# Kernel tuning notes

Hardware: AMD Instinct MI355X
Metric: run time of the kernel (lower is better)

The kernel has to match this reference:

```python
import jax, jax.numpy as jnp
import numpy as np

EPS = 1e-08

def setup_inputs() -> dict:
    key = jax.random.key(0)
    k1, k2, k3 = jax.random.split(key, 3)
    B, T, V = 16384, 512, 2
    outputs = jax.random.uniform(k1, (B, T, V), dtype=jnp.float32)
    targets = jax.random.uniform(k2, (B, T, V), dtype=jnp.float32)
    weights = jax.random.uniform(k3, (B, T), dtype=jnp.float32)
    return {"outputs": outputs, "targets": targets, "weights": weights}

def reference(outputs, targets, weights):
    # Faithful vectorization of the double python loop in CensoredLoss_Sub
    # (reduction='mean'). Original accumulates a length-D vector:
    #   loss += (t0 * log(1 - o) + t1 * log(o)) * w  over all (i, t)
    # then returns -loss / (B*T).
    B, T, V = targets.shape
    out = outputs.reshape(B, T, -1)                 # (B, T, D)
    loss1 = targets[:, :, 0:1] * jnp.log((1.0 - out) + EPS)
    loss2 = targets[:, :, 1:2] * jnp.log(out + EPS)
    total = (loss1 + loss2) * weights[:, :, None]   # (B, T, D)
    loss = jnp.sum(total, axis=(0, 1))              # (D,)
    return -loss / (B * T)
```

## Files before the change

kernel.cpp:

```cpp
#include <hip/hip_runtime.h>

#define EPS 1e-8f
#define NBLOCKS 2048
#define NTHREADS 256

__global__ __launch_bounds__(NTHREADS) void cl_partial(
    const float4* __restrict__ o4p,
    const float4* __restrict__ t4p,
    const float2* __restrict__ w2p,
    float* __restrict__ ws,
    int M)
{
    int tid = blockIdx.x * blockDim.x + threadIdx.x;
    int stride = gridDim.x * blockDim.x;

    float s0 = 0.0f, s1 = 0.0f;

    for (int j = tid; j < M; j += stride) {
        float4 o4 = o4p[j];
        float4 t4 = t4p[j];
        float2 w2 = w2p[j];

        float lA0m = __logf((1.0f - o4.x) + EPS);
        float lA0  = __logf(o4.x + EPS);
        float lA1m = __logf((1.0f - o4.y) + EPS);
        float lA1  = __logf(o4.y + EPS);
        s0 += (t4.x * lA0m + t4.y * lA0) * w2.x;
        s1 += (t4.x * lA1m + t4.y * lA1) * w2.x;

        float lB0m = __logf((1.0f - o4.z) + EPS);
        float lB0  = __logf(o4.z + EPS);
        float lB1m = __logf((1.0f - o4.w) + EPS);
        float lB1  = __logf(o4.w + EPS);
        s0 += (t4.z * lB0m + t4.w * lB0) * w2.y;
        s1 += (t4.z * lB1m + t4.w * lB1) * w2.y;
    }

    #pragma unroll
    for (int off = 32; off > 0; off >>= 1) {
        s0 += __shfl_down(s0, off, 64);
        s1 += __shfl_down(s1, off, 64);
    }

    __shared__ float sm[ (NTHREADS/64) * 2 ];
    int wave = threadIdx.x >> 6;
    int lane = threadIdx.x & 63;
    if (lane == 0) { sm[wave * 2 + 0] = s0; sm[wave * 2 + 1] = s1; }
    __syncthreads();

    if (threadIdx.x == 0) {
        float b0 = 0.0f, b1 = 0.0f;
        #pragma unroll
        for (int wv = 0; wv < NTHREADS / 64; ++wv) {
            b0 += sm[wv * 2 + 0];
            b1 += sm[wv * 2 + 1];
        }
        ws[blockIdx.x * 2 + 0] = b0;
        ws[blockIdx.x * 2 + 1] = b1;
    }
}

__global__ __launch_bounds__(NTHREADS) void cl_final(
    const float* __restrict__ ws,
    float* __restrict__ out,
    int nblocks,
    float invN)
{
    double s0 = 0.0, s1 = 0.0;
    for (int j = threadIdx.x; j < nblocks; j += NTHREADS) {
        s0 += (double)ws[j * 2 + 0];
        s1 += (double)ws[j * 2 + 1];
    }

    #pragma unroll
    for (int off = 32; off > 0; off >>= 1) {
        s0 += __shfl_down(s0, off, 64);
        s1 += __shfl_down(s1, off, 64);
    }

    __shared__ double sm[ (NTHREADS/64) * 2 ];
    int wave = threadIdx.x >> 6;
    int lane = threadIdx.x & 63;
    if (lane == 0) { sm[wave * 2 + 0] = s0; sm[wave * 2 + 1] = s1; }
    __syncthreads();

    if (threadIdx.x == 0) {
        double b0 = 0.0, b1 = 0.0;
        #pragma unroll
        for (int wv = 0; wv < NTHREADS / 64; ++wv) {
            b0 += sm[wv * 2 + 0];
            b1 += sm[wv * 2 + 1];
        }
        out[0] = (float)(-b0 * (double)invN);
        out[1] = (float)(-b1 * (double)invN);
    }
}

extern "C" void kernel_launch(void* const* d_in, const int* in_sizes, int n_in,
                              void* d_out, int out_size, void* d_ws, size_t ws_size,
                              hipStream_t stream) {
    const float* outputs = (const float*)d_in[0];
    const float* targets = (const float*)d_in[1];
    const float* weights = (const float*)d_in[2];

    int N = in_sizes[2];
    int M = N / 2;

    float* ws = (float*)d_ws;
    float* out = (float*)d_out;

    int nblocks = (M + NTHREADS - 1) / NTHREADS;
    if (nblocks > NBLOCKS) nblocks = NBLOCKS;

    cl_partial<<<nblocks, NTHREADS, 0, stream>>>(
        (const float4*)outputs, (const float4*)targets, (const float2*)weights,
        ws, M);

    cl_final<<<1, NTHREADS, 0, stream>>>(ws, out, nblocks, 1.0f / (float)N);
}
```

Measured before the change: 34.84 us.

## Use larger grid with two-item-per-thread fast path and upfront loads

Raises the grid cap so that each thread handles exactly two float4 groups. When the problem size matches, all six loads are issued up front behind a scheduling barrier, and the compute follows. Adds an occupancy hint and vectorized float2 reads in the final reduction. This is meant to increase memory-level parallelism and remove grid-stride loop overhead. The cost is more partial sums for the single-block final kernel to reduce.

```diff
diff --git a/kernel.cpp b/kernel.cpp
--- a/kernel.cpp
+++ b/kernel.cpp
@@ -1,39 +1,51 @@
 #include <hip/hip_runtime.h>
 
 #define EPS 1e-8f
-#define NBLOCKS 2048
+#define NBLOCKS 8192
 #define NTHREADS 256
 
-__global__ __launch_bounds__(NTHREADS) void cl_partial(
+__device__ __forceinline__ void accum_group(float4 o4, float4 t4, float2 w2,
+                                            float& s0, float& s1) {
+    float lA0m = __logf((1.0f - o4.x) + EPS);
+    float lA0  = __logf(o4.x + EPS);
+    float lA1m = __logf((1.0f - o4.y) + EPS);
+    float lA1  = __logf(o4.y + EPS);
+    s0 += (t4.x * lA0m + t4.y * lA0) * w2.x;
+    s1 += (t4.x * lA1m + t4.y * lA1) * w2.x;
+    float lB0m = __logf((1.0f - o4.z) + EPS);
+    float lB0  = __logf(o4.z + EPS);
+    float lB1m = __logf((1.0f - o4.w) + EPS);
+    float lB1  = __logf(o4.w + EPS);
+    s0 += (t4.z * lB0m + t4.w * lB0) * w2.y;
+    s1 += (t4.z * lB1m + t4.w * lB1) * w2.y;
+}
+
+__global__ __launch_bounds__(NTHREADS, 8) void cl_partial(
     const float4* __restrict__ o4p,
     const float4* __restrict__ t4p,
     const float2* __restrict__ w2p,
     float* __restrict__ ws,
     int M)
 {
-    int tid = blockIdx.x * blockDim.x + threadIdx.x;
-    int stride = gridDim.x * blockDim.x;
+    int tid = blockIdx.x * NTHREADS + threadIdx.x;
+    int stride = gridDim.x * NTHREADS;
 
     float s0 = 0.0f, s1 = 0.0f;
 
-    for (int j = tid; j < M; j += stride) {
-        float4 o4 = o4p[j];
-        float4 t4 = t4p[j];
-        float2 w2 = w2p[j];
-
-        float lA0m = __logf((1.0f - o4.x) + EPS);
-        float lA0  = __logf(o4.x + EPS);
-        float lA1m = __logf((1.0f - o4.y) + EPS);
-        float lA1  = __logf(o4.y + EPS);
-        s0 += (t4.x * lA0m + t4.y * lA0) * w2.x;
-        s1 += (t4.x * lA1m + t4.y * lA1) * w2.x;
-
-        float lB0m = __logf((1.0f - o4.z) + EPS);
-        float lB0  = __logf(o4.z + EPS);
-        float lB1m = __logf((1.0f - o4.w) + EPS);
-        float lB1  = __logf(o4.w + EPS);
-        s0 += (t4.z * lB0m + t4.w * lB0) * w2.y;
-        s1 += (t4.z * lB1m + t4.w * lB1) * w2.y;
+    if (M == 2 * stride) {
+        float4 oa = o4p[tid];
+        float4 ob = o4p[tid + stride];
+        float4 ta = t4p[tid];
+        float4 tb = t4p[tid + stride];
+        float2 wa = w2p[tid];
+        float2 wb = w2p[tid + stride];
+        __builtin_amdgcn_sched_barrier(0);
+        accum_group(oa, ta, wa, s0, s1);
+        accum_group(ob, tb, wb, s0, s1);
+    } else {
+        for (int j = tid; j < M; j += stride) {
+            accum_group(o4p[j], t4p[j], w2p[j], s0, s1);
+        }
     }
 
     #pragma unroll
@@ -42,7 +54,7 @@
         s1 += __shfl_down(s1, off, 64);
     }
 
-    __shared__ float sm[ (NTHREADS/64) * 2 ];
+    __shared__ float sm[(NTHREADS / 64) * 2];
     int wave = threadIdx.x >> 6;
     int lane = threadIdx.x & 63;
     if (lane == 0) { sm[wave * 2 + 0] = s0; sm[wave * 2 + 1] = s1; }
@@ -61,15 +73,16 @@
 }
 
 __global__ __launch_bounds__(NTHREADS) void cl_final(
-    const float* __restrict__ ws,
+    const float2* __restrict__ ws,
     float* __restrict__ out,
     int nblocks,
     float invN)
 {
     double s0 = 0.0, s1 = 0.0;
     for (int j = threadIdx.x; j < nblocks; j += NTHREADS) {
-        s0 += (double)ws[j * 2 + 0];
-        s1 += (double)ws[j * 2 + 1];
+        float2 p = ws[j];
+        s0 += (double)p.x;
+        s1 += (double)p.y;
     }
 
     #pragma unroll
@@ -78,7 +91,7 @@
         s1 += __shfl_down(s1, off, 64);
     }
 
-    __shared__ double sm[ (NTHREADS/64) * 2 ];
+    __shared__ double sm[(NTHREADS / 64) * 2];
     int wave = threadIdx.x >> 6;
     int lane = threadIdx.x & 63;
     if (lane == 0) { sm[wave * 2 + 0] = s0; sm[wave * 2 + 1] = s1; }
@@ -109,12 +122,15 @@
     float* ws = (float*)d_ws;
     float* out = (float*)d_out;
 
-    int nblocks = (M + NTHREADS - 1) / NTHREADS;
+    int nblocks = (M + 2 * NTHREADS - 1) / (2 * NTHREADS);
     if (nblocks > NBLOCKS) nblocks = NBLOCKS;
+    int max_by_ws = (int)(ws_size / (2 * sizeof(float)));
+    if (nblocks > max_by_ws) nblocks = max_by_ws;
 
     cl_partial<<<nblocks, NTHREADS, 0, stream>>>(
         (const float4*)outputs, (const float4*)targets, (const float2*)weights,
         ws, M);
 
-    cl_final<<<1, NTHREADS, 0, stream>>>(ws, out, nblocks, 1.0f / (float)N);
+    cl_final<<<1, NTHREADS, 0, stream>>>((const float2*)ws, out, nblocks,
+                                         1.0f / (float)N);
 }
```

Measured after the change: 40.39 us. 1.16x slower.
